# Performance work log

Measured on AMD Instinct MI355X. Metric: run time of the kernel, lower is better.

## Reference

```python
import jax, jax.numpy as jnp
import numpy as np
from jax import lax

BN_EPS = 1e-5

def _bn(x, g, b):
    # eval-mode BatchNorm with default running stats (mean=0, var=1)
    sh = (1, -1) + (1,) * (x.ndim - 2)
    return x * (g / jnp.sqrt(1.0 + BN_EPS)).reshape(sh) + b.reshape(sh)

def _simam(x, lam=1e-4):
    axes = tuple(range(2, x.ndim))
    mu = x.mean(axis=axes, keepdims=True)
    d2 = (x - mu) ** 2
    var = d2.mean(axis=axes, keepdims=True)
    e = d2 / (2.0 * var + 1e-12) + lam
    return jax.nn.sigmoid(1.0 / (e + 1e-12)) * x

def _dwconv1d(x, w, pad, groups):
    return lax.conv_general_dilated(
        x, w, (1,), [(pad, pad)],
        dimension_numbers=('NCH', 'OIH', 'NCH'),
        feature_group_count=groups)

def _adaptive_pool_matrix(t_in, t_out):
    # torch AdaptiveAvgPool1d: window i = [floor(i*t_in/t_out), ceil((i+1)*t_in/t_out))
    M = np.zeros((t_in, t_out), dtype=np.float32)
    for i in range(t_out):
        s = (i * t_in) // t_out
        e = -(-((i + 1) * t_in) // t_out)
        M[s:e, i] = 1.0 / (e - s)
    return jnp.asarray(M)

def _deform_conv1d(x, w, ow, ob):
    # depthwise deformable conv1d, padding='valid'; grid_sample bilinear,
    # zeros padding, align_corners=True -> pure 1D bilinear gather at pos.
    B, C, T = x.shape
    K = w.shape[1]
    T_out = T - K + 1
    off = _dwconv1d(x, ow, 0, C) + ob[None, :, None]        # (B, C*K, T_out)
    off = off.reshape(B, C, K, T_out)
    pos = (jnp.arange(T_out, dtype=x.dtype)[None, None, None, :]
           + jnp.arange(K, dtype=x.dtype)[None, None, :, None] + off)
    i0f = jnp.floor(pos)
    f = pos - i0f
    i0 = i0f.astype(jnp.int32)
    xb = jnp.broadcast_to(x[:, :, None, :], (B, C, K, T))
    def gather(idx):
        valid = (idx >= 0) & (idx < T)
        v = jnp.take_along_axis(xb, jnp.clip(idx, 0, T - 1), axis=3)
        return jnp.where(valid, v, 0.0)
    samp = gather(i0) * (1.0 - f) + gather(i0 + 1) * f      # (B,C,K,T_out)
    return jnp.einsum('bckt,ck->bct', samp, w)

def _branch(x, sw, g1, b1, tw, g2, b2):
    # spatial depthwise conv (kernel covers full channel axis) -> (B,5,T)
    h = jnp.einsum('bcht,ch->bct', x, sw)
    h = _simam(jax.nn.elu(_bn(h, g1, b1)))
    h = _dwconv1d(h, tw, tw.shape[-1] // 2, h.shape[1])     # temporal depthwise, same length
    return _simam(jax.nn.elu(_bn(h, g2, b2)))

def setup_inputs() -> dict:
    key = jax.random.key(0)
    ks = iter(jax.random.split(key, 48))
    B, C_in, T, n_class = 256, 22, 1000, 4
    k1, k2, k3 = 15, 31, 63  # _odd(round(fs*{0.06,0.12,0.25})), fs=250
    def rn(shape, scale=0.1):
        return scale * jax.random.normal(next(ks), shape, dtype=jnp.float32)
    inp = {'x': jax.random.normal(next(ks), (B, 1, C_in, T), dtype=jnp.float32),
           'stem_w': rn((15, 1, 2, 3)),
           'stem_g': 1.0 + rn((15,)), 'stem_b': rn((15,))}
    for i, kt in zip((1, 2, 3), (k1, k2, k3)):
        inp[f'b{i}_sw'] = rn((5, C_in))
        inp[f'b{i}_g1'] = 1.0 + rn((5,)); inp[f'b{i}_b1'] = rn((5,))
        inp[f'b{i}_tw'] = rn((5, 1, kt))
        inp[f'b{i}_g2'] = 1.0 + rn((5,)); inp[f'b{i}_b2'] = rn((5,))
    inp['pw_w'] = rn((5, 15))
    inp['pw_g'] = 1.0 + rn((5,)); inp['pw_b'] = rn((5,))
    inp['d1_w'] = rn((5, 5));  inp['d1_ow'] = rn((25, 1, 5), 0.02);  inp['d1_ob'] = jnp.zeros((25,), jnp.float32)
    inp['d2_w'] = rn((5, 10)); inp['d2_ow'] = rn((50, 1, 10), 0.02); inp['d2_ob'] = jnp.zeros((50,), jnp.float32)
    inp['fc_w'] = rn((n_class, 5 * 25)); inp['fc_b'] = rn((n_class,))
    return inp

def reference(x, stem_w, stem_g, stem_b,
              b1_sw, b1_g1, b1_b1, b1_tw, b1_g2, b1_b2,
              b2_sw, b2_g1, b2_b1, b2_tw, b2_g2, b2_b2,
              b3_sw, b3_g1, b3_b1, b3_tw, b3_g2, b3_b2,
              pw_w, pw_g, pw_b,
              d1_w, d1_ow, d1_ob, d2_w, d2_ow, d2_ob,
              fc_w, fc_b):
    # stem: conv2d k=(2,3) 'same' (torch pads extra on the right for even k)
    h = lax.conv_general_dilated(x, stem_w, (1, 1), [(0, 1), (1, 1)],
                                 dimension_numbers=('NCHW', 'OIHW', 'NCHW'))
    h = jax.nn.elu(_bn(h, stem_g, stem_b))                  # (B,15,22,T); dropout = eval no-op
    o1 = _branch(h[:, 0:5],  b1_sw, b1_g1, b1_b1, b1_tw, b1_g2, b1_b2)
    o2 = _branch(h[:, 5:10], b2_sw, b2_g1, b2_b1, b2_tw, b2_g2, b2_b2)
    o3 = _branch(h[:, 10:15], b3_sw, b3_g1, b3_b1, b3_tw, b3_g2, b3_b2)
    hc = jnp.concatenate([o1, o2, o3], axis=1)              # (B,15,T)
    hc = jnp.einsum('bct,to->bco', hc, _adaptive_pool_matrix(hc.shape[-1], 40))
    hc = jnp.einsum('bct,oc->bot', hc, pw_w)                # 1x1 pointwise
    hc = _simam(jax.nn.elu(_bn(hc, pw_g, pw_b)))            # (B,5,40)
    hc = _deform_conv1d(hc, d1_w, d1_ow, d1_ob)             # (B,5,36)
    hc = _deform_conv1d(hc, d2_w, d2_ow, d2_ob)             # (B,5,27)
    hc = jnp.einsum('bct,to->bco', hc, _adaptive_pool_matrix(hc.shape[-1], 25))
    return hc.reshape(hc.shape[0], -1) @ fc_w.T + fc_b      # (B,n_class)
```

## Files before the change

kernel.cpp:

```cpp
#include <hip/hip_runtime.h>
#include <math.h>

#define BNS 0.99999500003749972f

__device__ __forceinline__ float eluf(float v) {
    return v > 0.f ? v : (__expf(v) - 1.f);
}
__device__ __forceinline__ float sigmf(float u) {
    return 1.f / (1.f + __expf(-u));
}
__device__ __forceinline__ float sgpr(float v) {
    return __int_as_float(__builtin_amdgcn_readfirstlane(__float_as_int(v)));
}

#define PSTR 1024
#define PADZ 32
#define ZLEN 1120

__device__ __forceinline__ void block_reduce2(float& s1, float& s2, float* red) {
#pragma unroll
    for (int m = 32; m > 0; m >>= 1) {
        s1 += __shfl_xor(s1, m, 64);
        s2 += __shfl_xor(s2, m, 64);
    }
    const int wid = threadIdx.x >> 6, lane = threadIdx.x & 63;
    if (lane == 0) { red[wid * 2] = s1; red[wid * 2 + 1] = s2; }
    __syncthreads();
    s1 = red[0] + red[2] + red[4] + red[6];
    s2 = red[1] + red[3] + red[5] + red[7];
}

__global__ __launch_bounds__(512) void k_stem(
    const float* __restrict__ x,
    const float* __restrict__ stem_w,
    const float* __restrict__ stem_g, const float* __restrict__ stem_b,
    const float* __restrict__ sw1, const float* __restrict__ sw2, const float* __restrict__ sw3,
    float* __restrict__ pre)
{
    const int tid = threadIdx.x;
    const int lane = tid & 63;
    const int g = blockIdx.x;
    const int b = blockIdx.y;
    const float* xb = x + b * 22000;

    const float* swp = (g == 0 ? sw1 : g == 1 ? sw2 : sw3);
    float wrow[5];
#pragma unroll
    for (int c = 0; c < 5; ++c)
        wrow[c] = (lane < 22) ? swp[c * 22 + lane] : 0.f;

    if (tid >= 500) return;
    const int t0 = tid * 2;

    float w[5][6], bs[5];
#pragma unroll
    for (int c = 0; c < 5; ++c) {
        const int C = g * 5 + c;
        const float gsc = sgpr(stem_g[C]) * BNS;
#pragma unroll
        for (int j = 0; j < 6; ++j) w[c][j] = sgpr(stem_w[C * 6 + j]) * gsc;
        bs[c] = sgpr(stem_b[C]);
    }

    const bool sel0 = (t0 == 0), sel2 = (t0 == 998);
    const int base = sel0 ? 0 : (sel2 ? 996 : t0 - 1);

    float acc0[5] = {0.f, 0.f, 0.f, 0.f, 0.f};
    float acc1[5] = {0.f, 0.f, 0.f, 0.f, 0.f};

    #define LOADW(rp, w0, w1, w2, w3)                                   \
    {                                                                   \
        const float4 v = *reinterpret_cast<const float4*>((rp) + base); \
        w0 = sel0 ? 0.f : (sel2 ? v.y : v.x);                           \
        w1 = sel0 ? v.x : (sel2 ? v.z : v.y);                           \
        w2 = sel0 ? v.y : (sel2 ? v.w : v.z);                           \
        w3 = sel2 ? 0.f : (sel0 ? v.z : v.w);                           \
    }

    float c0, c1, c2, c3, n0, n1, n2, n3, p0, p1, p2, p3;
    LOADW(xb, c0, c1, c2, c3)
    LOADW(xb + 1000, n0, n1, n2, n3)

#pragma unroll 1
    for (int i = 0; i < 22; ++i) {
        if (i + 2 < 22) {
            LOADW(xb + (i + 2) * 1000, p0, p1, p2, p3)
        } else {
            p0 = p1 = p2 = p3 = 0.f;
        }
#pragma unroll
        for (int c = 0; c < 5; ++c) {
            const float sv = __shfl(wrow[c], i, 64);
            float v0 = fmaf(w[c][0], c0, fmaf(w[c][1], c1, fmaf(w[c][2], c2,
                       fmaf(w[c][3], n0, fmaf(w[c][4], n1, fmaf(w[c][5], n2, bs[c]))))));
            float v1 = fmaf(w[c][0], c1, fmaf(w[c][1], c2, fmaf(w[c][2], c3,
                       fmaf(w[c][3], n1, fmaf(w[c][4], n2, fmaf(w[c][5], n3, bs[c]))))));
            acc0[c] += eluf(v0) * sv;
            acc1[c] += eluf(v1) * sv;
        }
        c0 = n0; c1 = n1; c2 = n2; c3 = n3;
        n0 = p0; n1 = p1; n2 = p2; n3 = p3;
    }
    #undef LOADW

    float* prow0 = pre + (b * 15 + g * 5) * PSTR + t0;
#pragma unroll
    for (int c = 0; c < 5; ++c) {
        float2 o; o.x = acc0[c]; o.y = acc1[c];
        *reinterpret_cast<float2*>(prow0 + c * PSTR) = o;
    }
}

template<int K>
__device__ __forceinline__ void branch_block(
    const float* __restrict__ row,
    float g1s, float b1v,
    float wreg,
    float g2s, float b2v,
    float* __restrict__ zrow,
    float* __restrict__ red,
    float* __restrict__ out40)
{
    const int tid = threadIdx.x;
    const int t0 = tid * 4;
    const bool act = tid < 250;

    if (tid < PADZ) zrow[tid] = 0.f;
    if (tid >= 32 && tid < 120) zrow[PADZ + 1000 + (tid - 32)] = 0.f;

    float y0 = 0.f, y1 = 0.f, y2 = 0.f, y3 = 0.f, s1 = 0.f, s2 = 0.f;
    if (act) {
        const float4 v = *reinterpret_cast<const float4*>(row + t0);
        y0 = eluf(v.x * g1s + b1v);
        y1 = eluf(v.y * g1s + b1v);
        y2 = eluf(v.z * g1s + b1v);
        y3 = eluf(v.w * g1s + b1v);
        s1 = y0 + y1 + y2 + y3;
        s2 = y0 * y0 + y1 * y1 + y2 * y2 + y3 * y3;
    }
    block_reduce2(s1, s2, red);
    {
        const float mu = s1 * 1e-3f;
        const float var = s2 * 1e-3f - mu * mu;
        const float iv = 1.f / (2.f * var + 1e-12f);
        if (act) {
            float d;
            float4 z;
            d = y0 - mu; z.x = sigmf(1.f / (d * d * iv + 1e-4f + 1e-12f)) * y0;
            d = y1 - mu; z.y = sigmf(1.f / (d * d * iv + 1e-4f + 1e-12f)) * y1;
            d = y2 - mu; z.z = sigmf(1.f / (d * d * iv + 1e-4f + 1e-12f)) * y2;
            d = y3 - mu; z.w = sigmf(1.f / (d * d * iv + 1e-4f + 1e-12f)) * y3;
            *reinterpret_cast<float4*>(&zrow[PADZ + t0]) = z;
        }
    }
    __syncthreads();

    float a0 = 0.f, a1 = 0.f, a2 = 0.f, a3 = 0.f;
    if (act) {
        const int A = PADZ + t0 - (K / 2) - 1;
        float W[20];
#pragma unroll
        for (int q = 0; q < 5; ++q)
            *reinterpret_cast<float4*>(&W[q * 4]) = *reinterpret_cast<const float4*>(&zrow[A + q * 4]);

#pragma unroll
        for (int cb = 0; cb < K; cb += 16) {
            float P[16];
            if (cb + 16 < K) {
#pragma unroll
                for (int q = 0; q < 4; ++q)
                    *reinterpret_cast<float4*>(&P[q * 4]) =
                        *reinterpret_cast<const float4*>(&zrow[A + cb + 20 + q * 4]);
            }
            const int DD = (K - cb < 16) ? (K - cb) : 16;
#pragma unroll
            for (int dd = 0; dd < DD; ++dd) {
                const float wv = __shfl(wreg, cb + dd, 64);
                a0 += W[dd + 1] * wv;
                a1 += W[dd + 2] * wv;
                a2 += W[dd + 3] * wv;
                a3 += W[dd + 4] * wv;
            }
            if (cb + 16 < K) {
#pragma unroll
                for (int q = 0; q < 4; ++q) W[q] = W[16 + q];
#pragma unroll
                for (int q = 0; q < 16; ++q) W[4 + q] = P[q];
            }
        }
    }

    float u0 = 0.f, u1 = 0.f, u2 = 0.f, u3 = 0.f;
    s1 = 0.f; s2 = 0.f;
    if (act) {
        u0 = eluf(a0 * g2s + b2v);
        u1 = eluf(a1 * g2s + b2v);
        u2 = eluf(a2 * g2s + b2v);
        u3 = eluf(a3 * g2s + b2v);
        s1 = u0 + u1 + u2 + u3;
        s2 = u0 * u0 + u1 * u1 + u2 * u2 + u3 * u3;
    }
    block_reduce2(s1, s2, red);
    {
        const float mu = s1 * 1e-3f;
        const float var = s2 * 1e-3f - mu * mu;
        const float iv = 1.f / (2.f * var + 1e-12f);
        if (act) {
            float d;
            float4 z;
            d = u0 - mu; z.x = sigmf(1.f / (d * d * iv + 1e-4f + 1e-12f)) * u0;
            d = u1 - mu; z.y = sigmf(1.f / (d * d * iv + 1e-4f + 1e-12f)) * u1;
            d = u2 - mu; z.z = sigmf(1.f / (d * d * iv + 1e-4f + 1e-12f)) * u2;
            d = u3 - mu; z.w = sigmf(1.f / (d * d * iv + 1e-4f + 1e-12f)) * u3;
            *reinterpret_cast<float4*>(&zrow[PADZ + t0]) = z;
        }
    }
    __syncthreads();

    if (tid < 40) {
        float s = 0.f;
#pragma unroll
        for (int q = 0; q < 25; ++q) s += zrow[PADZ + tid * 25 + q];
        out40[tid] = s * (1.f / 25.f);
    }
}

__global__ __launch_bounds__(256) void k_branch(
    const float* __restrict__ pre,
    const float* __restrict__ g1a, const float* __restrict__ b1a,
    const float* __restrict__ tw1,
    const float* __restrict__ g2a, const float* __restrict__ b2a,
    const float* __restrict__ g1b, const float* __restrict__ b1b,
    const float* __restrict__ tw2,
    const float* __restrict__ g2b, const float* __restrict__ b2b,
    const float* __restrict__ g1c, const float* __restrict__ b1c,
    const float* __restrict__ tw3,
    const float* __restrict__ g2c, const float* __restrict__ b2c,
    float* __restrict__ pooled)
{
    __shared__ float zrow[ZLEN];
    __shared__ float red[8];

    const int row_id = blockIdx.x;
    const int C = row_id % 15;
    const int br = C / 5, c = C % 5;
    const int lane = threadIdx.x & 63;

    const float* row = pre + (size_t)row_id * PSTR;
    float* out40 = pooled + row_id * 40;

    if (br == 0) {
        const float wreg = (lane < 15) ? tw1[c * 15 + lane] : 0.f;
        branch_block<15>(row, g1a[c] * BNS, b1a[c], wreg, g2a[c] * BNS, b2a[c], zrow, red, out40);
    } else if (br == 1) {
        const float wreg = (lane < 31) ? tw2[c * 31 + lane] : 0.f;
        branch_block<31>(row, g1b[c] * BNS, b1b[c], wreg, g2b[c] * BNS, b2b[c], zrow, red, out40);
    } else {
        const float wreg = (lane < 63) ? tw3[c * 63 + lane] : 0.f;
        branch_block<63>(row, g1c[c] * BNS, b1c[c], wreg, g2c[c] * BNS, b2c[c], zrow, red, out40);
    }
}

__global__ __launch_bounds__(128) void k_head(
    const float* __restrict__ pooled,
    const float* __restrict__ pw_w, const float* __restrict__ pw_g, const float* __restrict__ pw_b,
    const float* __restrict__ d1_w, const float* __restrict__ d1_ow, const float* __restrict__ d1_ob,
    const float* __restrict__ d2_w, const float* __restrict__ d2_ow, const float* __restrict__ d2_ob,
    const float* __restrict__ fc_w, const float* __restrict__ fc_b,
    float* __restrict__ out)
{
    __shared__ float P[600];
    __shared__ float A[200];
    __shared__ float Bv[200];
    __shared__ float C1[180];
    __shared__ float C2[135];
    __shared__ float D[125];
    __shared__ float mu5[5], iv5[5];

    const int b = blockIdx.x, tid = threadIdx.x;

    for (int i = tid; i < 600; i += 128) P[i] = pooled[b * 600 + i];
    __syncthreads();

    for (int i = tid; i < 200; i += 128) {
        int o = i / 40, t = i % 40;
        float s = 0.f;
        for (int cc = 0; cc < 15; ++cc) s += P[cc * 40 + t] * pw_w[o * 15 + cc];
        float v = s * (pw_g[o] * BNS) + pw_b[o];
        A[i] = eluf(v);
    }
    __syncthreads();

    if (tid < 5) {
        float s = 0.f;
        for (int t = 0; t < 40; ++t) s += A[tid * 40 + t];
        float mu = s * (1.f / 40.f);
        float v2 = 0.f;
        for (int t = 0; t < 40; ++t) { float d = A[tid * 40 + t] - mu; v2 += d * d; }
        mu5[tid] = mu;
        iv5[tid] = 1.f / (2.f * (v2 * (1.f / 40.f)) + 1e-12f);
    }
    __syncthreads();

    for (int i = tid; i < 200; i += 128) {
        int o = i / 40;
        float a = A[i];
        float d = a - mu5[o];
        float e = d * d * iv5[o] + 1e-4f;
        Bv[i] = sigmf(1.f / (e + 1e-12f)) * a;
    }
    __syncthreads();

    for (int i = tid; i < 180; i += 128) {
        int cc = i / 36, t = i % 36;
        float o = 0.f;
        for (int k = 0; k < 5; ++k) {
            float off = d1_ob[cc * 5 + k];
            for (int d = 0; d < 5; ++d) off += Bv[cc * 40 + t + d] * d1_ow[(cc * 5 + k) * 5 + d];
            float pos = (float)(t + k) + off;
            float fl = floorf(pos);
            float f = pos - fl;
            int i0 = (int)fl;
            float v0 = (i0 >= 0 && i0 < 40) ? Bv[cc * 40 + i0] : 0.f;
            float v1 = (i0 + 1 >= 0 && i0 + 1 < 40) ? Bv[cc * 40 + i0 + 1] : 0.f;
            o += (v0 * (1.f - f) + v1 * f) * d1_w[cc * 5 + k];
        }
        C1[i] = o;
    }
    __syncthreads();

    for (int i = tid; i < 135; i += 128) {
        int cc = i / 27, t = i % 27;
        float o = 0.f;
        for (int k = 0; k < 10; ++k) {
            float off = d2_ob[cc * 10 + k];
            for (int d = 0; d < 10; ++d) off += C1[cc * 36 + t + d] * d2_ow[(cc * 10 + k) * 10 + d];
            float pos = (float)(t + k) + off;
            float fl = floorf(pos);
            float f = pos - fl;
            int i0 = (int)fl;
            float v0 = (i0 >= 0 && i0 < 36) ? C1[cc * 36 + i0] : 0.f;
            float v1 = (i0 + 1 >= 0 && i0 + 1 < 36) ? C1[cc * 36 + i0 + 1] : 0.f;
            o += (v0 * (1.f - f) + v1 * f) * d2_w[cc * 10 + k];
        }
        C2[i] = o;
    }
    __syncthreads();

    for (int i = tid; i < 125; i += 128) {
        int cc = i / 25, j = i % 25;
        int s0 = (j * 27) / 25;
        int e0 = ((j + 1) * 27 + 24) / 25;
        float s = 0.f;
        for (int q = s0; q < e0; ++q) s += C2[cc * 27 + q];
        D[i] = s / (float)(e0 - s0);
    }
    __syncthreads();

    if (tid < 64) {
        float part0 = 0.f, part1 = 0.f, part2 = 0.f, part3 = 0.f;
        for (int i = tid; i < 125; i += 64) {
            const float dv = D[i];
            part0 += dv * fc_w[0 * 125 + i];
            part1 += dv * fc_w[1 * 125 + i];
            part2 += dv * fc_w[2 * 125 + i];
            part3 += dv * fc_w[3 * 125 + i];
        }
#pragma unroll
        for (int m = 32; m > 0; m >>= 1) {
            part0 += __shfl_xor(part0, m, 64);
            part1 += __shfl_xor(part1, m, 64);
            part2 += __shfl_xor(part2, m, 64);
            part3 += __shfl_xor(part3, m, 64);
        }
        if (tid == 0) {
            out[b * 4 + 0] = part0 + fc_b[0];
            out[b * 4 + 1] = part1 + fc_b[1];
            out[b * 4 + 2] = part2 + fc_b[2];
            out[b * 4 + 3] = part3 + fc_b[3];
        }
    }
}

extern "C" void kernel_launch(void* const* d_in, const int* in_sizes, int n_in,
                              void* d_out, int out_size, void* d_ws, size_t ws_size,
                              hipStream_t stream) {
    const float* x      = (const float*)d_in[0];
    const float* stem_w = (const float*)d_in[1];
    const float* stem_g = (const float*)d_in[2];
    const float* stem_b = (const float*)d_in[3];
    const float* b1_sw = (const float*)d_in[4];
    const float* b1_g1 = (const float*)d_in[5];
    const float* b1_b1 = (const float*)d_in[6];
    const float* b1_tw = (const float*)d_in[7];
    const float* b1_g2 = (const float*)d_in[8];
    const float* b1_b2 = (const float*)d_in[9];
    const float* b2_sw = (const float*)d_in[10];
    const float* b2_g1 = (const float*)d_in[11];
    const float* b2_b1 = (const float*)d_in[12];
    const float* b2_tw = (const float*)d_in[13];
    const float* b2_g2 = (const float*)d_in[14];
    const float* b2_b2 = (const float*)d_in[15];
    const float* b3_sw = (const float*)d_in[16];
    const float* b3_g1 = (const float*)d_in[17];
    const float* b3_b1 = (const float*)d_in[18];
    const float* b3_tw = (const float*)d_in[19];
    const float* b3_g2 = (const float*)d_in[20];
    const float* b3_b2 = (const float*)d_in[21];
    const float* pw_w  = (const float*)d_in[22];
    const float* pw_g  = (const float*)d_in[23];
    const float* pw_b  = (const float*)d_in[24];
    const float* d1_w  = (const float*)d_in[25];
    const float* d1_ow = (const float*)d_in[26];
    const float* d1_ob = (const float*)d_in[27];
    const float* d2_w  = (const float*)d_in[28];
    const float* d2_ow = (const float*)d_in[29];
    const float* d2_ob = (const float*)d_in[30];
    const float* fc_w  = (const float*)d_in[31];
    const float* fc_b  = (const float*)d_in[32];

    float* pre    = (float*)d_ws;
    float* pooled = (float*)((char*)d_ws + (size_t)256 * 15 * PSTR * 4);

    k_stem<<<dim3(3, 256), 512, 0, stream>>>(
        x, stem_w, stem_g, stem_b, b1_sw, b2_sw, b3_sw, pre);

    k_branch<<<3840, 256, 0, stream>>>(
        pre,
        b1_g1, b1_b1, b1_tw, b1_g2, b1_b2,
        b2_g1, b2_b1, b2_tw, b2_g2, b2_b2,
        b3_g1, b3_b1, b3_tw, b3_g2, b3_b2,
        pooled);

    k_head<<<256, 128, 0, stream>>>(
        pooled, pw_w, pw_g, pw_b,
        d1_w, d1_ow, d1_ob, d2_w, d2_ow, d2_ob,
        fc_w, fc_b, (float*)d_out);
}
```

Baseline: 76.88 us.

## Fuse stem and branch kernels, keeping stem output in shared memory

Merges the stem convolution kernel and the per-row branch kernel into one kernel per (group, batch). The stem results for the five channels are kept in LDS, and each block then processes its five branch rows sequentially. This removes the global write and read of the intermediate buffer and one kernel launch. In exchange, the branch stage runs with far fewer blocks and serial per-row loops, each with several block barriers, which reduces parallelism.

```diff
diff --git a/kernel.cpp b/kernel.cpp
--- a/kernel.cpp
+++ b/kernel.cpp
@@ -13,11 +13,10 @@
     return __int_as_float(__builtin_amdgcn_readfirstlane(__float_as_int(v)));
 }
 
-#define PSTR 1024
 #define PADZ 32
-#define ZLEN 1120
-
-__device__ __forceinline__ void block_reduce2(float& s1, float& s2, float* red) {
+#define ZLEN 1140
+
+__device__ __forceinline__ void block_reduce2_8(float& s1, float& s2, float* red) {
 #pragma unroll
     for (int m = 32; m > 0; m >>= 1) {
         s1 += __shfl_xor(s1, m, 64);
@@ -26,207 +25,112 @@
     const int wid = threadIdx.x >> 6, lane = threadIdx.x & 63;
     if (lane == 0) { red[wid * 2] = s1; red[wid * 2 + 1] = s2; }
     __syncthreads();
-    s1 = red[0] + red[2] + red[4] + red[6];
-    s2 = red[1] + red[3] + red[5] + red[7];
-}
-
-__global__ __launch_bounds__(512) void k_stem(
+    s1 = red[0] + red[2] + red[4] + red[6] + red[8] + red[10] + red[12] + red[14];
+    s2 = red[1] + red[3] + red[5] + red[7] + red[9] + red[11] + red[13] + red[15];
+}
+
+template<int K>
+__device__ __forceinline__ void branch_rows(
+    const float* __restrict__ preL,
+    const float* __restrict__ g1p, const float* __restrict__ b1p,
+    const float* __restrict__ twp,
+    const float* __restrict__ g2p, const float* __restrict__ b2p,
+    float* __restrict__ zrow,
+    float* __restrict__ red,
+    float* __restrict__ out)
+{
+    const int tid = threadIdx.x;
+    const int lane = tid & 63;
+    const bool act = tid < 500;
+    const int t0 = tid * 2;
+
+    for (int r = 0; r < 5; ++r) {
+        const float g1s = sgpr(g1p[r]) * BNS, b1v = sgpr(b1p[r]);
+        const float g2s = sgpr(g2p[r]) * BNS, b2v = sgpr(b2p[r]);
+        const float wreg = (lane < K) ? twp[r * K + lane] : 0.f;
+
+        float y0 = 0.f, y1 = 0.f, s1 = 0.f, s2 = 0.f;
+        if (act) {
+            const float2 v = *reinterpret_cast<const float2*>(&preL[r * 1000 + t0]);
+            y0 = eluf(v.x * g1s + b1v);
+            y1 = eluf(v.y * g1s + b1v);
+            s1 = y0 + y1;
+            s2 = y0 * y0 + y1 * y1;
+        }
+        block_reduce2_8(s1, s2, red);
+        {
+            const float mu = s1 * 1e-3f;
+            const float var = s2 * 1e-3f - mu * mu;
+            const float iv = 1.f / (2.f * var + 1e-12f);
+            if (act) {
+                float d;
+                float2 z;
+                d = y0 - mu; z.x = sigmf(1.f / (d * d * iv + 1e-4f + 1e-12f)) * y0;
+                d = y1 - mu; z.y = sigmf(1.f / (d * d * iv + 1e-4f + 1e-12f)) * y1;
+                *reinterpret_cast<float2*>(&zrow[PADZ + t0]) = z;
+            }
+        }
+        __syncthreads();
+
+        float a0 = 0.f, a1 = 0.f;
+        if (act) {
+            const int A = PADZ + t0 - (K / 2) - 1;
+#pragma unroll
+            for (int cb = 0; cb < K; cb += 16) {
+                const int DD = (K - cb < 16) ? (K - cb) : 16;
+                const int RD = (DD + 3) & ~1;
+                float W[20];
+#pragma unroll
+                for (int q = 0; q < RD / 2; ++q)
+                    *reinterpret_cast<float2*>(&W[2 * q]) =
+                        *reinterpret_cast<const float2*>(&zrow[A + cb + 2 * q]);
+#pragma unroll
+                for (int j = 0; j < DD; ++j) {
+                    const float wv = __shfl(wreg, cb + j, 64);
+                    a0 += W[j + 1] * wv;
+                    a1 += W[j + 2] * wv;
+                }
+            }
+        }
+
+        float u0 = 0.f, u1 = 0.f;
+        s1 = 0.f; s2 = 0.f;
+        if (act) {
+            u0 = eluf(a0 * g2s + b2v);
+            u1 = eluf(a1 * g2s + b2v);
+            s1 = u0 + u1;
+            s2 = u0 * u0 + u1 * u1;
+        }
+        block_reduce2_8(s1, s2, red);
+        {
+            const float mu = s1 * 1e-3f;
+            const float var = s2 * 1e-3f - mu * mu;
+            const float iv = 1.f / (2.f * var + 1e-12f);
+            if (act) {
+                float d;
+                float2 z;
+                d = u0 - mu; z.x = sigmf(1.f / (d * d * iv + 1e-4f + 1e-12f)) * u0;
+                d = u1 - mu; z.y = sigmf(1.f / (d * d * iv + 1e-4f + 1e-12f)) * u1;
+                *reinterpret_cast<float2*>(&zrow[PADZ + t0]) = z;
+            }
+        }
+        __syncthreads();
+
+        if (tid < 40) {
+            float s = 0.f;
+#pragma unroll
+            for (int q = 0; q < 25; ++q) s += zrow[PADZ + tid * 25 + q];
+            out[r * 40 + tid] = s * (1.f / 25.f);
+        }
+        __syncthreads();
+    }
+}
+
+__global__ __launch_bounds__(512) void k_fused(
     const float* __restrict__ x,
     const float* __restrict__ stem_w,
     const float* __restrict__ stem_g, const float* __restrict__ stem_b,
     const float* __restrict__ sw1, const float* __restrict__ sw2, const float* __restrict__ sw3,
-    float* __restrict__ pre)
-{
-    const int tid = threadIdx.x;
-    const int lane = tid & 63;
-    const int g = blockIdx.x;
-    const int b = blockIdx.y;
-    const float* xb = x + b * 22000;
-
-    const float* swp = (g == 0 ? sw1 : g == 1 ? sw2 : sw3);
-    float wrow[5];
-#pragma unroll
-    for (int c = 0; c < 5; ++c)
-        wrow[c] = (lane < 22) ? swp[c * 22 + lane] : 0.f;
-
-    if (tid >= 500) return;
-    const int t0 = tid * 2;
-
-    float w[5][6], bs[5];
-#pragma unroll
-    for (int c = 0; c < 5; ++c) {
-        const int C = g * 5 + c;
-        const float gsc = sgpr(stem_g[C]) * BNS;
-#pragma unroll
-        for (int j = 0; j < 6; ++j) w[c][j] = sgpr(stem_w[C * 6 + j]) * gsc;
-        bs[c] = sgpr(stem_b[C]);
-    }
-
-    const bool sel0 = (t0 == 0), sel2 = (t0 == 998);
-    const int base = sel0 ? 0 : (sel2 ? 996 : t0 - 1);
-
-    float acc0[5] = {0.f, 0.f, 0.f, 0.f, 0.f};
-    float acc1[5] = {0.f, 0.f, 0.f, 0.f, 0.f};
-
-    #define LOADW(rp, w0, w1, w2, w3)                                   \
-    {                                                                   \
-        const float4 v = *reinterpret_cast<const float4*>((rp) + base); \
-        w0 = sel0 ? 0.f : (sel2 ? v.y : v.x);                           \
-        w1 = sel0 ? v.x : (sel2 ? v.z : v.y);                           \
-        w2 = sel0 ? v.y : (sel2 ? v.w : v.z);                           \
-        w3 = sel2 ? 0.f : (sel0 ? v.z : v.w);                           \
-    }
-
-    float c0, c1, c2, c3, n0, n1, n2, n3, p0, p1, p2, p3;
-    LOADW(xb, c0, c1, c2, c3)
-    LOADW(xb + 1000, n0, n1, n2, n3)
-
-#pragma unroll 1
-    for (int i = 0; i < 22; ++i) {
-        if (i + 2 < 22) {
-            LOADW(xb + (i + 2) * 1000, p0, p1, p2, p3)
-        } else {
-            p0 = p1 = p2 = p3 = 0.f;
-        }
-#pragma unroll
-        for (int c = 0; c < 5; ++c) {
-            const float sv = __shfl(wrow[c], i, 64);
-            float v0 = fmaf(w[c][0], c0, fmaf(w[c][1], c1, fmaf(w[c][2], c2,
-                       fmaf(w[c][3], n0, fmaf(w[c][4], n1, fmaf(w[c][5], n2, bs[c]))))));
-            float v1 = fmaf(w[c][0], c1, fmaf(w[c][1], c2, fmaf(w[c][2], c3,
-                       fmaf(w[c][3], n1, fmaf(w[c][4], n2, fmaf(w[c][5], n3, bs[c]))))));
-            acc0[c] += eluf(v0) * sv;
-            acc1[c] += eluf(v1) * sv;
-        }
-        c0 = n0; c1 = n1; c2 = n2; c3 = n3;
-        n0 = p0; n1 = p1; n2 = p2; n3 = p3;
-    }
-    #undef LOADW
-
-    float* prow0 = pre + (b * 15 + g * 5) * PSTR + t0;
-#pragma unroll
-    for (int c = 0; c < 5; ++c) {
-        float2 o; o.x = acc0[c]; o.y = acc1[c];
-        *reinterpret_cast<float2*>(prow0 + c * PSTR) = o;
-    }
-}
-
-template<int K>
-__device__ __forceinline__ void branch_block(
-    const float* __restrict__ row,
-    float g1s, float b1v,
-    float wreg,
-    float g2s, float b2v,
-    float* __restrict__ zrow,
-    float* __restrict__ red,
-    float* __restrict__ out40)
-{
-    const int tid = threadIdx.x;
-    const int t0 = tid * 4;
-    const bool act = tid < 250;
-
-    if (tid < PADZ) zrow[tid] = 0.f;
-    if (tid >= 32 && tid < 120) zrow[PADZ + 1000 + (tid - 32)] = 0.f;
-
-    float y0 = 0.f, y1 = 0.f, y2 = 0.f, y3 = 0.f, s1 = 0.f, s2 = 0.f;
-    if (act) {
-        const float4 v = *reinterpret_cast<const float4*>(row + t0);
-        y0 = eluf(v.x * g1s + b1v);
-        y1 = eluf(v.y * g1s + b1v);
-        y2 = eluf(v.z * g1s + b1v);
-        y3 = eluf(v.w * g1s + b1v);
-        s1 = y0 + y1 + y2 + y3;
-        s2 = y0 * y0 + y1 * y1 + y2 * y2 + y3 * y3;
-    }
-    block_reduce2(s1, s2, red);
-    {
-        const float mu = s1 * 1e-3f;
-        const float var = s2 * 1e-3f - mu * mu;
-        const float iv = 1.f / (2.f * var + 1e-12f);
-        if (act) {
-            float d;
-            float4 z;
-            d = y0 - mu; z.x = sigmf(1.f / (d * d * iv + 1e-4f + 1e-12f)) * y0;
-            d = y1 - mu; z.y = sigmf(1.f / (d * d * iv + 1e-4f + 1e-12f)) * y1;
-            d = y2 - mu; z.z = sigmf(1.f / (d * d * iv + 1e-4f + 1e-12f)) * y2;
-            d = y3 - mu; z.w = sigmf(1.f / (d * d * iv + 1e-4f + 1e-12f)) * y3;
-            *reinterpret_cast<float4*>(&zrow[PADZ + t0]) = z;
-        }
-    }
-    __syncthreads();
-
-    float a0 = 0.f, a1 = 0.f, a2 = 0.f, a3 = 0.f;
-    if (act) {
-        const int A = PADZ + t0 - (K / 2) - 1;
-        float W[20];
-#pragma unroll
-        for (int q = 0; q < 5; ++q)
-            *reinterpret_cast<float4*>(&W[q * 4]) = *reinterpret_cast<const float4*>(&zrow[A + q * 4]);
-
-#pragma unroll
-        for (int cb = 0; cb < K; cb += 16) {
-            float P[16];
-            if (cb + 16 < K) {
-#pragma unroll
-                for (int q = 0; q < 4; ++q)
-                    *reinterpret_cast<float4*>(&P[q * 4]) =
-                        *reinterpret_cast<const float4*>(&zrow[A + cb + 20 + q * 4]);
-            }
-            const int DD = (K - cb < 16) ? (K - cb) : 16;
-#pragma unroll
-            for (int dd = 0; dd < DD; ++dd) {
-                const float wv = __shfl(wreg, cb + dd, 64);
-                a0 += W[dd + 1] * wv;
-                a1 += W[dd + 2] * wv;
-                a2 += W[dd + 3] * wv;
-                a3 += W[dd + 4] * wv;
-            }
-            if (cb + 16 < K) {
-#pragma unroll
-                for (int q = 0; q < 4; ++q) W[q] = W[16 + q];
-#pragma unroll
-                for (int q = 0; q < 16; ++q) W[4 + q] = P[q];
-            }
-        }
-    }
-
-    float u0 = 0.f, u1 = 0.f, u2 = 0.f, u3 = 0.f;
-    s1 = 0.f; s2 = 0.f;
-    if (act) {
-        u0 = eluf(a0 * g2s + b2v);
-        u1 = eluf(a1 * g2s + b2v);
-        u2 = eluf(a2 * g2s + b2v);
-        u3 = eluf(a3 * g2s + b2v);
-        s1 = u0 + u1 + u2 + u3;
-        s2 = u0 * u0 + u1 * u1 + u2 * u2 + u3 * u3;
-    }
-    block_reduce2(s1, s2, red);
-    {
-        const float mu = s1 * 1e-3f;
-        const float var = s2 * 1e-3f - mu * mu;
-        const float iv = 1.f / (2.f * var + 1e-12f);
-        if (act) {
-            float d;
-            float4 z;
-            d = u0 - mu; z.x = sigmf(1.f / (d * d * iv + 1e-4f + 1e-12f)) * u0;
-            d = u1 - mu; z.y = sigmf(1.f / (d * d * iv + 1e-4f + 1e-12f)) * u1;
-            d = u2 - mu; z.z = sigmf(1.f / (d * d * iv + 1e-4f + 1e-12f)) * u2;
-            d = u3 - mu; z.w = sigmf(1.f / (d * d * iv + 1e-4f + 1e-12f)) * u3;
-            *reinterpret_cast<float4*>(&zrow[PADZ + t0]) = z;
-        }
-    }
-    __syncthreads();
-
-    if (tid < 40) {
-        float s = 0.f;
-#pragma unroll
-        for (int q = 0; q < 25; ++q) s += zrow[PADZ + tid * 25 + q];
-        out40[tid] = s * (1.f / 25.f);
-    }
-}
-
-__global__ __launch_bounds__(256) void k_branch(
-    const float* __restrict__ pre,
     const float* __restrict__ g1a, const float* __restrict__ b1a,
     const float* __restrict__ tw1,
     const float* __restrict__ g2a, const float* __restrict__ b2a,
@@ -238,26 +142,94 @@
     const float* __restrict__ g2c, const float* __restrict__ b2c,
     float* __restrict__ pooled)
 {
+    __shared__ float preL[5000];
     __shared__ float zrow[ZLEN];
-    __shared__ float red[8];
-
-    const int row_id = blockIdx.x;
-    const int C = row_id % 15;
-    const int br = C / 5, c = C % 5;
-    const int lane = threadIdx.x & 63;
-
-    const float* row = pre + (size_t)row_id * PSTR;
-    float* out40 = pooled + row_id * 40;
-
-    if (br == 0) {
-        const float wreg = (lane < 15) ? tw1[c * 15 + lane] : 0.f;
-        branch_block<15>(row, g1a[c] * BNS, b1a[c], wreg, g2a[c] * BNS, b2a[c], zrow, red, out40);
-    } else if (br == 1) {
-        const float wreg = (lane < 31) ? tw2[c * 31 + lane] : 0.f;
-        branch_block<31>(row, g1b[c] * BNS, b1b[c], wreg, g2b[c] * BNS, b2b[c], zrow, red, out40);
+    __shared__ float red[16];
+
+    const int tid = threadIdx.x;
+    const int lane = tid & 63;
+    const int g = blockIdx.x;
+    const int b = blockIdx.y;
+    const float* xb = x + b * 22000;
+
+    const float* swp = (g == 0 ? sw1 : g == 1 ? sw2 : sw3);
+    float wrow[5];
+#pragma unroll
+    for (int c = 0; c < 5; ++c)
+        wrow[c] = (lane < 22) ? swp[c * 22 + lane] : 0.f;
+
+    if (tid < 500) {
+        const int t0 = tid * 2;
+
+        float w[5][6], bs[5];
+#pragma unroll
+        for (int c = 0; c < 5; ++c) {
+            const int C = g * 5 + c;
+            const float gsc = sgpr(stem_g[C]) * BNS;
+#pragma unroll
+            for (int j = 0; j < 6; ++j) w[c][j] = sgpr(stem_w[C * 6 + j]) * gsc;
+            bs[c] = sgpr(stem_b[C]);
+        }
+
+        const bool sel0 = (t0 == 0), sel2 = (t0 == 998);
+        const int base = sel0 ? 0 : (sel2 ? 996 : t0 - 1);
+
+        float acc0[5] = {0.f, 0.f, 0.f, 0.f, 0.f};
+        float acc1[5] = {0.f, 0.f, 0.f, 0.f, 0.f};
+
+        #define LOADW(rp, w0, w1, w2, w3)                                   \
+        {                                                                   \
+            const float4 v = *reinterpret_cast<const float4*>((rp) + base); \
+            w0 = sel0 ? 0.f : (sel2 ? v.y : v.x);                           \
+            w1 = sel0 ? v.x : (sel2 ? v.z : v.y);                           \
+            w2 = sel0 ? v.y : (sel2 ? v.w : v.z);                           \
+            w3 = sel2 ? 0.f : (sel0 ? v.z : v.w);                           \
+        }
+
+        float c0, c1, c2, c3, n0, n1, n2, n3, p0, p1, p2, p3;
+        LOADW(xb, c0, c1, c2, c3)
+        LOADW(xb + 1000, n0, n1, n2, n3)
+
+#pragma unroll 1
+        for (int i = 0; i < 22; ++i) {
+            if (i + 2 < 22) {
+                LOADW(xb + (i + 2) * 1000, p0, p1, p2, p3)
+            } else {
+                p0 = p1 = p2 = p3 = 0.f;
+            }
+#pragma unroll
+            for (int c = 0; c < 5; ++c) {
+                const float sv = __shfl(wrow[c], i, 64);
+                float v0 = fmaf(w[c][0], c0, fmaf(w[c][1], c1, fmaf(w[c][2], c2,
+                           fmaf(w[c][3], n0, fmaf(w[c][4], n1, fmaf(w[c][5], n2, bs[c]))))));
+                float v1 = fmaf(w[c][0], c1, fmaf(w[c][1], c2, fmaf(w[c][2], c3,
+                           fmaf(w[c][3], n1, fmaf(w[c][4], n2, fmaf(w[c][5], n3, bs[c]))))));
+                acc0[c] += eluf(v0) * sv;
+                acc1[c] += eluf(v1) * sv;
+            }
+            c0 = n0; c1 = n1; c2 = n2; c3 = n3;
+            n0 = p0; n1 = p1; n2 = p2; n3 = p3;
+        }
+        #undef LOADW
+
+#pragma unroll
+        for (int c = 0; c < 5; ++c) {
+            float2 o; o.x = acc0[c]; o.y = acc1[c];
+            *reinterpret_cast<float2*>(&preL[c * 1000 + t0]) = o;
+        }
+    }
+
+    if (tid < PADZ) zrow[tid] = 0.f;
+    if (tid >= 32 && tid < 140) zrow[PADZ + 1000 + (tid - 32)] = 0.f;
+    __syncthreads();
+
+    float* out = pooled + (b * 15 + g * 5) * 40;
+    if (g == 0) {
+        branch_rows<15>(preL, g1a, b1a, tw1, g2a, b2a, zrow, red, out);
+    } else if (g == 1) {
+        branch_rows<31>(preL, g1b, b1b, tw2, g2b, b2b, zrow, red, out);
     } else {
-        const float wreg = (lane < 63) ? tw3[c * 63 + lane] : 0.f;
-        branch_block<63>(row, g1c[c] * BNS, b1c[c], wreg, g2c[c] * BNS, b2c[c], zrow, red, out40);
+        branch_rows<63>(preL, g1c, b1c, tw3, g2c, b2c, zrow, red, out);
     }
 }
 
@@ -419,14 +391,10 @@
     const float* fc_w  = (const float*)d_in[31];
     const float* fc_b  = (const float*)d_in[32];
 
-    float* pre    = (float*)d_ws;
-    float* pooled = (float*)((char*)d_ws + (size_t)256 * 15 * PSTR * 4);
-
-    k_stem<<<dim3(3, 256), 512, 0, stream>>>(
-        x, stem_w, stem_g, stem_b, b1_sw, b2_sw, b3_sw, pre);
-
-    k_branch<<<3840, 256, 0, stream>>>(
-        pre,
+    float* pooled = (float*)d_ws;
+
+    k_fused<<<dim3(3, 256), 512, 0, stream>>>(
+        x, stem_w, stem_g, stem_b, b1_sw, b2_sw, b3_sw,
         b1_g1, b1_b1, b1_tw, b1_g2, b1_b2,
         b2_g1, b2_b1, b2_tw, b2_g2, b2_b2,
         b3_g1, b3_b1, b3_tw, b3_g2, b3_b2,
```

Result: slower. 82.79 us (+7.7%).
